# Kernel optimization log

Hardware: AMD Instinct MI355X
Metric: run time of the kernel (lower is better)

Reference implementation:

```python
import jax, jax.numpy as jnp
import numpy as np

EPS = 1e-6

def setup_inputs() -> dict:
    key = jax.random.key(0)
    k1, k2, k3, k4 = jax.random.split(key, 4)
    B, H, S, D1, D2 = 2, 8, 2048, 128, 128
    q = jax.random.normal(k1, (B, H, S, D1), dtype=jnp.float32)
    k = jax.random.normal(k2, (B, H, S, D1), dtype=jnp.float32)
    v = jax.random.normal(k3, (B, H, S, D2), dtype=jnp.float32)
    omask = jax.random.uniform(k4, (1, H, S, S), dtype=jnp.float32)
    return {"q": q, "k": k, "v": v, "omask": omask}

def reference(q, k, v, omask):
    # normalize decay mask: mask_ij / sqrt(sum_j mask_ij), nan -> 0, drop leading dim
    mask = omask * jax.lax.rsqrt(jnp.sum(omask, axis=-1, keepdims=True))
    mask = jnp.nan_to_num(mask, nan=0.0)[0]  # [H, S1, S2]
    # scores: [B,H,S1,S2] = (q @ k^T) * mask, then contract with v
    scores = jnp.einsum('bhia,bhja->bhij', q, k) * mask[None]
    out = jnp.einsum('bhij,bhjc->bhic', scores, v)  # [B,H,S1,D2]
    # RMSNorm over last dim (no learned scale)
    out = out * jax.lax.rsqrt(jnp.mean(out * out, axis=-1, keepdims=True) + EPS)
    return out
```

## Files before the change

kernel.cpp:

```cpp
#include <hip/hip_runtime.h>

typedef unsigned short u16;
typedef __attribute__((ext_vector_type(4)))  unsigned int u32x4;
typedef __attribute__((ext_vector_type(4)))  float        f32x4;
typedef __attribute__((ext_vector_type(4)))  u16          u16x4;
typedef __attribute__((ext_vector_type(8)))  __bf16       bf16x8;
typedef __attribute__((ext_vector_type(16))) float        f32x16;

#define NB 2
#define NH 8
#define NS 2048
#define ND 128

static __device__ __forceinline__ u16 f2b(float x) {
  return __builtin_bit_cast(u16, (__bf16)x);
}

__global__ __launch_bounds__(256) void cvt_f32_bf16(const float* __restrict__ src,
                                                    u16* __restrict__ dst, int n4) {
  int i = blockIdx.x * 256 + threadIdx.x;
  if (i >= n4) return;
  f32x4 v = ((const f32x4*)src)[i];
  u16x4 o;
  o[0] = f2b(v[0]); o[1] = f2b(v[1]); o[2] = f2b(v[2]); o[3] = f2b(v[3]);
  ((u16x4*)dst)[i] = o;
}

__global__ __launch_bounds__(256) void vtrans(const float* __restrict__ v,
                                              u16* __restrict__ vt) {
  __shared__ u16 Lt[128][40];
  const int bh = blockIdx.y;
  const int s0 = blockIdx.x * 32;
  const int t  = threadIdx.x;
  const float* src = v + (size_t)(bh * NS + s0) * ND;
  const int srow = t >> 3;
#pragma unroll
  for (int it = 0; it < 4; ++it) {
    int c4 = (t & 7) + 8 * it;
    f32x4 x = *(const f32x4*)(src + srow * ND + c4 * 4);
#pragma unroll
    for (int jj = 0; jj < 4; ++jj) Lt[c4 * 4 + jj][srow] = f2b(x[jj]);
  }
  __syncthreads();
  const int d = t >> 1, sh = t & 1;
  u32x4 a  = *(const u32x4*)&Lt[d][sh * 16];
  u32x4 bq = *(const u32x4*)&Lt[d][sh * 16 + 8];
  u16* dst = vt + (size_t)(bh * ND + d) * NS + s0 + sh * 16;
  *(u32x4*)dst       = a;
  *(u32x4*)(dst + 8) = bq;
}

static __device__ __forceinline__ void gll16(u16* l, const u16* g) {
  __builtin_amdgcn_global_load_lds((const __attribute__((address_space(1))) void*)g,
                                   (__attribute__((address_space(3))) void*)l, 16, 0, 0);
}

__global__ __launch_bounds__(512, 2) void retention_main(
    const u16* __restrict__ qb, const u16* __restrict__ kb, const u16* __restrict__ vt,
    const float* __restrict__ omask, float* __restrict__ out) {
  __shared__ u16 Kls[2][2][2][32][128];
  __shared__ u16 Vls[2][2][2][128][32];
  __shared__ u16 Pls[8][32][32];

  const int tid  = threadIdx.x;
  const int w    = tid >> 6;
  const int lane = tid & 63;
  const int l31  = lane & 31;
  const int hh   = lane >> 5;

  const int h  = blockIdx.x & 7;
  const int qt = blockIdx.x >> 3;
  const int q0 = qt * 64;

  const int b  = w >> 2;
  const int r  = (w >> 1) & 1;
  const int jp = w & 1;

  const int sjp  = w & 1;
  const int sb   = (w >> 1) & 1;
  const int half = (w >> 2) & 1;

  bf16x8 qf[8];
  {
    const u16* qrow = qb + ((size_t)((b * NH + h) * NS) + q0 + r * 32 + l31) * ND;
#pragma unroll
    for (int ka = 0; ka < 8; ++ka)
      qf[ka] = __builtin_bit_cast(bf16x8, *(const u32x4*)(qrow + ka * 16 + hh * 8));
  }

  f32x16 acc[4];
#pragma unroll
  for (int n = 0; n < 4; ++n)
#pragma unroll
    for (int i = 0; i < 16; ++i) acc[n][i] = 0.0f;

  float mA[16], mB[16];

  auto STAGE = [&](int step, int db) {
    const int T = 2 * step + sjp;
    const u16* kg = kb + ((size_t)((sb * NH + h) * NS) + T * 32) * ND;
    u16* kl = &Kls[db][sjp][sb][0][0];
#pragma unroll
    for (int i = 0; i < 4; ++i) {
      int r0 = half * 16 + i * 4;
      int jr = r0 + (lane >> 4);
      int cc = (lane & 15) ^ (jr & 15);
      gll16(kl + r0 * 128, kg + jr * 128 + cc * 8);
    }
    const u16* vg = vt + (size_t)((sb * NH + h) * ND) * NS + T * 32;
    u16* vl = &Vls[db][sjp][sb][0][0];
#pragma unroll
    for (int i = 0; i < 4; ++i) {
      int r0 = half * 64 + i * 16;
      int rr = r0 + (lane >> 2);
      int cc = (lane & 3) ^ (rr & 3);
      gll16(vl + r0 * 32, vg + (size_t)rr * NS + cc * 8);
    }
  };

  auto LOADM = [&](float (&m)[16], int step) {
    const int T = 2 * step + jp;
    const float* mrow = omask + (size_t)h * NS * NS + (size_t)(q0 + r * 32) * NS + T * 32 + l31;
#pragma unroll
    for (int r16 = 0; r16 < 16; ++r16) {
      int qrow = (r16 & 3) + 8 * (r16 >> 2) + 4 * hh;
      m[r16] = mrow[(size_t)qrow * NS];
    }
  };

  auto COMPUTE = [&](int db, float (&m)[16]) {
    const u16* Kt = &Kls[db][jp][b][0][0];
    const u16* Vw = &Vls[db][jp][b][0][0];
    f32x16 s;
#pragma unroll
    for (int i = 0; i < 16; ++i) s[i] = 0.0f;
#pragma unroll
    for (int ka = 0; ka < 8; ++ka) {
      int cc = (2 * ka + hh) ^ (l31 & 15);
      bf16x8 kf = __builtin_bit_cast(bf16x8, *(const u32x4*)(Kt + l31 * 128 + cc * 8));
      s = __builtin_amdgcn_mfma_f32_32x32x16_bf16(qf[ka], kf, s, 0, 0, 0);
    }
    u16* Pw = &Pls[w][0][0];
#pragma unroll
    for (int r16 = 0; r16 < 16; ++r16) {
      int qrow = (r16 & 3) + 8 * (r16 >> 2) + 4 * hh;
      int idx  = qrow * 32 + (l31 ^ ((((qrow) >> 1) & 3) << 3));
      Pw[idx] = f2b(s[r16] * m[r16]);
    }
    asm volatile("" ::: "memory");
    bf16x8 pa[2];
#pragma unroll
    for (int kk = 0; kk < 2; ++kk) {
      int idx = l31 * 32 + ((8 * hh + 16 * kk) ^ (((l31 >> 1) & 3) << 3));
      pa[kk] = __builtin_bit_cast(bf16x8, *(const u32x4*)(Pw + idx));
    }
#pragma unroll
    for (int n = 0; n < 4; ++n) {
#pragma unroll
      for (int kk = 0; kk < 2; ++kk) {
        int cc = (2 * kk + hh) ^ (l31 & 3);
        bf16x8 vf = __builtin_bit_cast(bf16x8, *(const u32x4*)(Vw + (n * 32 + l31) * 32 + cc * 8));
        acc[n] = __builtin_amdgcn_mfma_f32_32x32x16_bf16(pa[kk], vf, acc[n], 0, 0, 0);
      }
    }
  };

  STAGE(0, 0);
  LOADM(mA, 0);
  __syncthreads();
  for (int it = 0; it < 16; ++it) {
    STAGE(2 * it + 1, 1);
    LOADM(mB, 2 * it + 1);
    COMPUTE(0, mA);
    __syncthreads();
    if (it < 15) { STAGE(2 * it + 2, 0); LOADM(mA, 2 * it + 2); }
    COMPUTE(1, mB);
    __syncthreads();
  }

  float* red = (float*)&Kls[0][0][0][0][0];
  const int wbr = b * 2 + r;
  if (jp == 1) {
#pragma unroll
    for (int n = 0; n < 4; ++n)
#pragma unroll
      for (int r16 = 0; r16 < 16; ++r16) {
        int qrow = (r16 & 3) + 8 * (r16 >> 2) + 4 * hh;
        red[(size_t)(wbr * 32 + qrow) * 128 + n * 32 + l31] = acc[n][r16];
      }
  }
  __syncthreads();
  if (jp == 0) {
#pragma unroll
    for (int n = 0; n < 4; ++n)
#pragma unroll
      for (int r16 = 0; r16 < 16; ++r16) {
        int qrow = (r16 & 3) + 8 * (r16 >> 2) + 4 * hh;
        acc[n][r16] += red[(size_t)(wbr * 32 + qrow) * 128 + n * 32 + l31];
      }
    float ss[16];
#pragma unroll
    for (int r16 = 0; r16 < 16; ++r16) {
      float t = 0.0f;
#pragma unroll
      for (int n = 0; n < 4; ++n) t += acc[n][r16] * acc[n][r16];
      ss[r16] = t;
    }
#pragma unroll
    for (int msk = 1; msk <= 16; msk <<= 1)
#pragma unroll
      for (int r16 = 0; r16 < 16; ++r16) ss[r16] += __shfl_xor(ss[r16], msk);
#pragma unroll
    for (int r16 = 0; r16 < 16; ++r16)
      ss[r16] = rsqrtf(ss[r16] * (1.0f / 128.0f) + 1e-6f);
    float* orow = out + ((size_t)((b * NH + h) * NS) + q0 + r * 32) * ND;
#pragma unroll
    for (int n = 0; n < 4; ++n)
#pragma unroll
      for (int r16 = 0; r16 < 16; ++r16) {
        int qrow = (r16 & 3) + 8 * (r16 >> 2) + 4 * hh;
        orow[(size_t)qrow * ND + n * 32 + l31] = acc[n][r16] * ss[r16];
      }
  }
}

extern "C" void kernel_launch(void* const* d_in, const int* in_sizes, int n_in,
                              void* d_out, int out_size, void* d_ws, size_t ws_size,
                              hipStream_t stream) {
  const float* q  = (const float*)d_in[0];
  const float* k  = (const float*)d_in[1];
  const float* v  = (const float*)d_in[2];
  const float* om = (const float*)d_in[3];
  float* out = (float*)d_out;

  const int NELT = NB * NH * NS * ND;
  u16* qb = (u16*)d_ws;
  u16* kb = qb + NELT;
  u16* vt = kb + NELT;

  const int n4 = NELT / 4;
  cvt_f32_bf16<<<n4 / 256, 256, 0, stream>>>(q, qb, n4);
  cvt_f32_bf16<<<n4 / 256, 256, 0, stream>>>(k, kb, n4);
  vtrans<<<dim3(NS / 32, NB * NH), 256, 0, stream>>>(v, vt);
  retention_main<<<256, 512, 0, stream>>>(qb, kb, vt, om, out);
}
```

Before: 286.3 us.

## Restructure retention kernel: per-batch blocks, fused prepass, in-kernel Q conversion

Each 256-thread block now owns one batch and a 128-row query tile, iterating over all 64 key tiles alone. This removes the split-j partial-sum reduction through shared memory but means the mask is no longer shared across the two batches, so each mask tile is read twice. The K conversion and V transpose are merged into a single prepass launch, and Q is converted to bf16 in registers inside the main kernel, dropping one launch and one workspace round trip. The grid stays at 256 blocks with half the threads each, so occupancy per CU changes and mask bandwidth doubles.

```diff
diff --git a/kernel.cpp b/kernel.cpp
--- a/kernel.cpp
+++ b/kernel.cpp
@@ -4,6 +4,7 @@
 typedef __attribute__((ext_vector_type(4)))  unsigned int u32x4;
 typedef __attribute__((ext_vector_type(4)))  float        f32x4;
 typedef __attribute__((ext_vector_type(4)))  u16          u16x4;
+typedef __attribute__((ext_vector_type(8)))  u16          u16x8;
 typedef __attribute__((ext_vector_type(8)))  __bf16       bf16x8;
 typedef __attribute__((ext_vector_type(16))) float        f32x16;
 
@@ -16,22 +17,23 @@
   return __builtin_bit_cast(u16, (__bf16)x);
 }
 
-__global__ __launch_bounds__(256) void cvt_f32_bf16(const float* __restrict__ src,
-                                                    u16* __restrict__ dst, int n4) {
-  int i = blockIdx.x * 256 + threadIdx.x;
-  if (i >= n4) return;
-  f32x4 v = ((const f32x4*)src)[i];
-  u16x4 o;
-  o[0] = f2b(v[0]); o[1] = f2b(v[1]); o[2] = f2b(v[2]); o[3] = f2b(v[3]);
-  ((u16x4*)dst)[i] = o;
-}
-
-__global__ __launch_bounds__(256) void vtrans(const float* __restrict__ v,
-                                              u16* __restrict__ vt) {
+__global__ __launch_bounds__(256) void prepass(const float* __restrict__ k,
+                                               const float* __restrict__ v,
+                                               u16* __restrict__ kb, u16* __restrict__ vt) {
+  const int bid = blockIdx.x;
+  const int t = threadIdx.x;
+  if (bid < 4096) {
+    int i = bid * 256 + t;
+    f32x4 x = ((const f32x4*)k)[i];
+    u16x4 o;
+    o[0] = f2b(x[0]); o[1] = f2b(x[1]); o[2] = f2b(x[2]); o[3] = f2b(x[3]);
+    ((u16x4*)kb)[i] = o;
+    return;
+  }
   __shared__ u16 Lt[128][40];
-  const int bh = blockIdx.y;
-  const int s0 = blockIdx.x * 32;
-  const int t  = threadIdx.x;
+  const int vb = bid - 4096;
+  const int bh = vb >> 6;
+  const int s0 = (vb & 63) * 32;
   const float* src = v + (size_t)(bh * NS + s0) * ND;
   const int srow = t >> 3;
 #pragma unroll
@@ -55,12 +57,12 @@
                                    (__attribute__((address_space(3))) void*)l, 16, 0, 0);
 }
 
-__global__ __launch_bounds__(512, 2) void retention_main(
-    const u16* __restrict__ qb, const u16* __restrict__ kb, const u16* __restrict__ vt,
+__global__ __launch_bounds__(256, 4) void retention_main(
+    const float* __restrict__ qf32, const u16* __restrict__ kb, const u16* __restrict__ vt,
     const float* __restrict__ omask, float* __restrict__ out) {
-  __shared__ u16 Kls[2][2][2][32][128];
-  __shared__ u16 Vls[2][2][2][128][32];
-  __shared__ u16 Pls[8][32][32];
+  __shared__ u16 Kls[2][32][128];
+  __shared__ u16 Vls[2][128][32];
+  __shared__ u16 Pls[4][32][32];
 
   const int tid  = threadIdx.x;
   const int w    = tid >> 6;
@@ -69,23 +71,23 @@
   const int hh   = lane >> 5;
 
   const int h  = blockIdx.x & 7;
-  const int qt = blockIdx.x >> 3;
-  const int q0 = qt * 64;
-
-  const int b  = w >> 2;
-  const int r  = (w >> 1) & 1;
-  const int jp = w & 1;
-
-  const int sjp  = w & 1;
-  const int sb   = (w >> 1) & 1;
-  const int half = (w >> 2) & 1;
+  const int b  = (blockIdx.x >> 3) & 1;
+  const int qt = blockIdx.x >> 4;
+  const int q0 = qt * 128;
+  const int qw = q0 + w * 32;
 
   bf16x8 qf[8];
   {
-    const u16* qrow = qb + ((size_t)((b * NH + h) * NS) + q0 + r * 32 + l31) * ND;
-#pragma unroll
-    for (int ka = 0; ka < 8; ++ka)
-      qf[ka] = __builtin_bit_cast(bf16x8, *(const u32x4*)(qrow + ka * 16 + hh * 8));
+    const float* qrow = qf32 + ((size_t)((b * NH + h) * NS) + qw + l31) * ND + hh * 8;
+#pragma unroll
+    for (int ka = 0; ka < 8; ++ka) {
+      f32x4 x0 = *(const f32x4*)(qrow + ka * 16);
+      f32x4 x1 = *(const f32x4*)(qrow + ka * 16 + 4);
+      u16x8 o;
+      o[0] = f2b(x0[0]); o[1] = f2b(x0[1]); o[2] = f2b(x0[2]); o[3] = f2b(x0[3]);
+      o[4] = f2b(x1[0]); o[5] = f2b(x1[1]); o[6] = f2b(x1[2]); o[7] = f2b(x1[3]);
+      qf[ka] = __builtin_bit_cast(bf16x8, o);
+    }
   }
 
   f32x16 acc[4];
@@ -94,33 +96,34 @@
 #pragma unroll
     for (int i = 0; i < 16; ++i) acc[n][i] = 0.0f;
 
-  float mA[16], mB[16];
-
-  auto STAGE = [&](int step, int db) {
-    const int T = 2 * step + sjp;
-    const u16* kg = kb + ((size_t)((sb * NH + h) * NS) + T * 32) * ND;
-    u16* kl = &Kls[db][sjp][sb][0][0];
-#pragma unroll
-    for (int i = 0; i < 4; ++i) {
-      int r0 = half * 16 + i * 4;
+  const u16* kg0 = kb + (size_t)((b * NH + h) * NS) * ND;
+  const u16* vg0 = vt + (size_t)((b * NH + h) * ND) * NS;
+  const float* mrow0 = omask + (size_t)h * NS * NS + (size_t)qw * NS;
+
+  auto STAGE = [&](int T, int db) {
+    const u16* kg = kg0 + (size_t)T * 32 * ND;
+    u16* kl = &Kls[db][0][0];
+#pragma unroll
+    for (int i = 0; i < 2; ++i) {
+      int r0 = w * 8 + i * 4;
       int jr = r0 + (lane >> 4);
       int cc = (lane & 15) ^ (jr & 15);
       gll16(kl + r0 * 128, kg + jr * 128 + cc * 8);
     }
-    const u16* vg = vt + (size_t)((sb * NH + h) * ND) * NS + T * 32;
-    u16* vl = &Vls[db][sjp][sb][0][0];
-#pragma unroll
-    for (int i = 0; i < 4; ++i) {
-      int r0 = half * 64 + i * 16;
+    const u16* vg = vg0 + T * 32;
+    u16* vl = &Vls[db][0][0];
+#pragma unroll
+    for (int i = 0; i < 2; ++i) {
+      int r0 = w * 32 + i * 16;
       int rr = r0 + (lane >> 2);
       int cc = (lane & 3) ^ (rr & 3);
       gll16(vl + r0 * 32, vg + (size_t)rr * NS + cc * 8);
     }
   };
 
-  auto LOADM = [&](float (&m)[16], int step) {
-    const int T = 2 * step + jp;
-    const float* mrow = omask + (size_t)h * NS * NS + (size_t)(q0 + r * 32) * NS + T * 32 + l31;
+  float m[16];
+  auto LOADM = [&](int T) {
+    const float* mrow = mrow0 + T * 32 + l31;
 #pragma unroll
     for (int r16 = 0; r16 < 16; ++r16) {
       int qrow = (r16 & 3) + 8 * (r16 >> 2) + 4 * hh;
@@ -128,9 +131,9 @@
     }
   };
 
-  auto COMPUTE = [&](int db, float (&m)[16]) {
-    const u16* Kt = &Kls[db][jp][b][0][0];
-    const u16* Vw = &Vls[db][jp][b][0][0];
+  auto COMPUTE = [&](int db) {
+    const u16* Kt = &Kls[db][0][0];
+    const u16* Vw = &Vls[db][0][0];
     f32x16 s;
 #pragma unroll
     for (int i = 0; i < 16; ++i) s[i] = 0.0f;
@@ -144,7 +147,7 @@
 #pragma unroll
     for (int r16 = 0; r16 < 16; ++r16) {
       int qrow = (r16 & 3) + 8 * (r16 >> 2) + 4 * hh;
-      int idx  = qrow * 32 + (l31 ^ ((((qrow) >> 1) & 3) << 3));
+      int idx  = qrow * 32 + (l31 ^ (((qrow >> 1) & 3) << 3));
       Pw[idx] = f2b(s[r16] * m[r16]);
     }
     asm volatile("" ::: "memory");
@@ -166,62 +169,39 @@
   };
 
   STAGE(0, 0);
-  LOADM(mA, 0);
   __syncthreads();
-  for (int it = 0; it < 16; ++it) {
-    STAGE(2 * it + 1, 1);
-    LOADM(mB, 2 * it + 1);
-    COMPUTE(0, mA);
+#pragma unroll 1
+  for (int t = 0; t < 64; ++t) {
+    int cur = t & 1;
+    LOADM(t);
+    if (t < 63) STAGE(t + 1, cur ^ 1);
+    COMPUTE(cur);
     __syncthreads();
-    if (it < 15) { STAGE(2 * it + 2, 0); LOADM(mA, 2 * it + 2); }
-    COMPUTE(1, mB);
-    __syncthreads();
-  }
-
-  float* red = (float*)&Kls[0][0][0][0][0];
-  const int wbr = b * 2 + r;
-  if (jp == 1) {
-#pragma unroll
-    for (int n = 0; n < 4; ++n)
-#pragma unroll
-      for (int r16 = 0; r16 < 16; ++r16) {
-        int qrow = (r16 & 3) + 8 * (r16 >> 2) + 4 * hh;
-        red[(size_t)(wbr * 32 + qrow) * 128 + n * 32 + l31] = acc[n][r16];
-      }
-  }
-  __syncthreads();
-  if (jp == 0) {
-#pragma unroll
-    for (int n = 0; n < 4; ++n)
-#pragma unroll
-      for (int r16 = 0; r16 < 16; ++r16) {
-        int qrow = (r16 & 3) + 8 * (r16 >> 2) + 4 * hh;
-        acc[n][r16] += red[(size_t)(wbr * 32 + qrow) * 128 + n * 32 + l31];
-      }
-    float ss[16];
+  }
+
+  float ss[16];
+#pragma unroll
+  for (int r16 = 0; r16 < 16; ++r16) {
+    float tt = 0.0f;
+#pragma unroll
+    for (int n = 0; n < 4; ++n) tt += acc[n][r16] * acc[n][r16];
+    ss[r16] = tt;
+  }
+#pragma unroll
+  for (int msk = 1; msk <= 16; msk <<= 1)
+#pragma unroll
+    for (int r16 = 0; r16 < 16; ++r16) ss[r16] += __shfl_xor(ss[r16], msk);
+#pragma unroll
+  for (int r16 = 0; r16 < 16; ++r16)
+    ss[r16] = rsqrtf(ss[r16] * (1.0f / 128.0f) + 1e-6f);
+  float* orow = out + ((size_t)((b * NH + h) * NS) + qw) * ND;
+#pragma unroll
+  for (int n = 0; n < 4; ++n)
 #pragma unroll
     for (int r16 = 0; r16 < 16; ++r16) {
-      float t = 0.0f;
-#pragma unroll
-      for (int n = 0; n < 4; ++n) t += acc[n][r16] * acc[n][r16];
-      ss[r16] = t;
-    }
-#pragma unroll
-    for (int msk = 1; msk <= 16; msk <<= 1)
-#pragma unroll
-      for (int r16 = 0; r16 < 16; ++r16) ss[r16] += __shfl_xor(ss[r16], msk);
-#pragma unroll
-    for (int r16 = 0; r16 < 16; ++r16)
-      ss[r16] = rsqrtf(ss[r16] * (1.0f / 128.0f) + 1e-6f);
-    float* orow = out + ((size_t)((b * NH + h) * NS) + q0 + r * 32) * ND;
-#pragma unroll
-    for (int n = 0; n < 4; ++n)
-#pragma unroll
-      for (int r16 = 0; r16 < 16; ++r16) {
-        int qrow = (r16 & 3) + 8 * (r16 >> 2) + 4 * hh;
-        orow[(size_t)qrow * ND + n * 32 + l31] = acc[n][r16] * ss[r16];
-      }
-  }
+      int qrow = (r16 & 3) + 8 * (r16 >> 2) + 4 * hh;
+      orow[(size_t)qrow * ND + n * 32 + l31] = acc[n][r16] * ss[r16];
+    }
 }
 
 extern "C" void kernel_launch(void* const* d_in, const int* in_sizes, int n_in,
@@ -234,13 +214,9 @@
   float* out = (float*)d_out;
 
   const int NELT = NB * NH * NS * ND;
-  u16* qb = (u16*)d_ws;
-  u16* kb = qb + NELT;
-  u16* vt = kb + NELT;
-
-  const int n4 = NELT / 4;
-  cvt_f32_bf16<<<n4 / 256, 256, 0, stream>>>(q, qb, n4);
-  cvt_f32_bf16<<<n4 / 256, 256, 0, stream>>>(k, kb, n4);
-  vtrans<<<dim3(NS / 32, NB * NH), 256, 0, stream>>>(v, vt);
-  retention_main<<<256, 512, 0, stream>>>(qb, kb, vt, om, out);
-}
+  u16* kbuf = (u16*)d_ws;
+  u16* vtb  = kbuf + NELT;
+
+  prepass<<<4096 + 1024, 256, 0, stream>>>(k, v, kbuf, vtb);
+  retention_main<<<256, 256, 0, stream>>>(q, kbuf, vtb, om, out);
+}
```

After: 707.0 us. +146.9%, slower.
